# Kernel tuning notes

Hardware: AMD Instinct MI355X
Metric: run time of the kernel (lower is better)

Reference implementation:

```python
import jax, jax.numpy as jnp
import numpy as np

N, E, F, H, L, G = 100000, 1600000, 32, 64, 4, 256
EPS = 1e-5


def setup_inputs() -> dict:
    key = jax.random.key(0)
    ks = jax.random.split(key, 12)
    x = jax.random.normal(ks[0], (N, F), dtype=jnp.float32)
    edge_index = jax.random.randint(ks[1], (2, E), 0, N, dtype=jnp.int32)
    batch = jnp.sort(jax.random.randint(ks[2], (N,), 0, G, dtype=jnp.int32))
    s = 0.1
    return {
        "x": x,
        "edge_index": edge_index,
        "batch": batch,
        "w_embed": jax.random.normal(ks[3], (F, H), dtype=jnp.float32) * s,
        "b_embed": jnp.zeros((H,), dtype=jnp.float32),
        "conv_W": jax.random.normal(ks[4], (L, H, H), dtype=jnp.float32) * s,
        "conv_b": jnp.zeros((L, H), dtype=jnp.float32),
        "bn_gamma": jnp.ones((L, H), dtype=jnp.float32),
        "bn_beta": jnp.zeros((L, H), dtype=jnp.float32),
        "w1": jax.random.normal(ks[5], (H, H // 2), dtype=jnp.float32) * s,
        "b1": jnp.zeros((H // 2,), dtype=jnp.float32),
        "w2": jax.random.normal(ks[6], (H // 2, 1), dtype=jnp.float32) * s,
        "b2": jnp.zeros((1,), dtype=jnp.float32),
    }


def _gcn_conv(h, src, dst, W, b):
    # PyG GCNConv: add self loops, symmetric D^-1/2 (A+I) D^-1/2 normalization
    hw = h @ W  # [N,H]
    deg = jax.ops.segment_sum(jnp.ones((E,), h.dtype), dst, num_segments=N) + 1.0
    dinv = jax.lax.rsqrt(deg)  # [N]
    msg = hw[src] * (dinv[src] * dinv[dst])[:, None]  # [E,H] gather + scale
    agg = jax.ops.segment_sum(msg, dst, num_segments=N)  # scatter-add
    agg = agg + hw * (dinv * dinv)[:, None]  # self-loop contribution
    return agg + b


def _batchnorm(h, gamma, beta):
    # training-mode BatchNorm1d over the node dimension
    mean = jnp.mean(h, axis=0)
    var = jnp.var(h, axis=0)
    return (h - mean) * jax.lax.rsqrt(var + EPS) * gamma + beta


def reference(x, edge_index, batch, w_embed, b_embed, conv_W, conv_b,
              bn_gamma, bn_beta, w1, b1, w2, b2):
    src, dst = edge_index[0], edge_index[1]
    h = x @ w_embed + b_embed  # node embedding [N,H]
    for i in range(L):
        identity = h
        h = _gcn_conv(h, src, dst, conv_W[i], conv_b[i])
        h = _batchnorm(h, bn_gamma[i], bn_beta[i])
        h = jax.nn.relu(h)
        # dropout is identity in eval mode
        h = h + identity  # use_residual=True
    # global mean pool over graphs
    sums = jax.ops.segment_sum(h, batch, num_segments=G)  # [G,H]
    counts = jax.ops.segment_sum(jnp.ones((N,), h.dtype), batch, num_segments=G)
    pooled = sums / jnp.maximum(counts, 1.0)[:, None]
    out = jax.nn.relu(pooled @ w1 + b1)
    out = out @ w2 + b2  # [G,1]
    return out
```

## Files before the change

kernel.cpp:

```cpp
#include <hip/hip_runtime.h>
#include <hip/hip_fp16.h>

#define Nn 100000
#define Ne 1600000
#define Fi 32
#define Hd 64
#define Ll 4
#define Gg 256
#define BN_EPS 1e-5f
#define NPB 128
#define NBINS ((Nn + NPB - 1) / NPB)
#define CHUNK 4096
#define NBLK ((Ne + CHUNK - 1) / CHUNK)
#define IDXW (NBINS + 2)
#define BSLOT 4096
#define TPAD 68
#define XPAD 36
#define NGB ((Nn + 63) / 64)
#define NSH 128


__global__ __launch_bounds__(256) void k_part(const int* __restrict__ src,
                                              const int* __restrict__ dst,
                                              unsigned* __restrict__ tpack,
                                              unsigned short* __restrict__ idx16) {
    __shared__ int hist[NBINS];
    __shared__ int lofs[NBINS + 1];
    __shared__ int wsum[256];
    __shared__ unsigned stage[CHUNK];
    int blk = blockIdx.x, t = threadIdx.x;
    int e0 = blk * CHUNK;
    int nval = min(CHUNK, Ne - e0);

    for (int i = t; i < NBINS; i += 256) hist[i] = 0;
    __syncthreads();
    for (int i = t; i < nval; i += 256)
        atomicAdd(&hist[dst[e0 + i] >> 7], 1);
    __syncthreads();

    int base = t * 4;
    int loc[4];
    int s = 0;
#pragma unroll
    for (int k = 0; k < 4; k++) {
        int b = base + k;
        int c = (b < NBINS) ? hist[b] : 0;
        loc[k] = s;
        s += c;
    }
    wsum[t] = s;
    __syncthreads();
    int x = s;
    for (int off = 1; off < 256; off <<= 1) {
        int u = (t >= off) ? wsum[t - off] : 0;
        __syncthreads();
        x += u;
        wsum[t] = x;
        __syncthreads();
    }
    int excl = x - s;
#pragma unroll
    for (int k = 0; k < 4; k++) {
        int b = base + k;
        if (b < NBINS) lofs[b] = excl + loc[k];
    }
    if (t == 0) lofs[NBINS] = nval;
    __syncthreads();

    for (int i = t; i <= NBINS; i += 256)
        idx16[(size_t)blk * IDXW + i] = (unsigned short)lofs[i];

    for (int i = t; i < NBINS; i += 256) hist[i] = lofs[i];
    __syncthreads();
    for (int i = t; i < nval; i += 256) {
        int d = dst[e0 + i];
        int sv = src[e0 + i];
        int p = atomicAdd(&hist[d >> 7], 1);
        stage[p] = (unsigned)sv | ((unsigned)(d & (NPB - 1)) << 17);
    }
    __syncthreads();
    for (int i = t; i < nval; i += 256)
        tpack[(size_t)blk * CHUNK + i] = stage[i];
}

__global__ __launch_bounds__(512) void k_csr2(const unsigned* __restrict__ tpack,
                                              const unsigned short* __restrict__ idx16,
                                              const int* __restrict__ batch,
                                              int* __restrict__ esrc,
                                              int* __restrict__ row_off,
                                              int* __restrict__ rdeg,
                                              float* __restrict__ dinv,
                                              int* __restrict__ gstart) {
    int t = threadIdx.x;
    if (blockIdx.x == NBINS) {
        if (t < Gg) {
            int lo = 0, hi = Nn;
            while (lo < hi) {
                int mid = (lo + hi) >> 1;
                if (batch[mid] < t) lo = mid + 1; else hi = mid;
            }
            gstart[t] = lo;
            if (t == 0) gstart[Gg] = Nn;
        }
        return;
    }
    __shared__ unsigned edges[BSLOT];
    __shared__ unsigned ordered[BSLOT];
    __shared__ int rlen[512];
    __shared__ int cnt[NPB], startv[NPB], cur[NPB];
    int b = blockIdx.x;
    int n0 = b * NPB;
    int base = b * BSLOT;

    int len = 0, s0 = 0;
    if (t < NBLK) {
        const unsigned short* row = idx16 + (size_t)t * IDXW;
        s0 = row[b];
        len = (int)row[b + 1] - s0;
    }
    rlen[t] = len;
    __syncthreads();
    int x = len;
    for (int off = 1; off < 512; off <<= 1) {
        int u = (t >= off) ? rlen[t - off] : 0;
        __syncthreads();
        x += u;
        rlen[t] = x;
        __syncthreads();
    }
    int lput = x - len;
    int total = rlen[511];
    if (t < NBLK && len > 0) {
        const unsigned* tp = tpack + (size_t)t * CHUNK + s0;
        for (int k = 0; k < len; k++)
            edges[lput + k] = tp[k];
    }
    if (t < NPB) cnt[t] = 0;
    __syncthreads();
    for (int i = t; i < total; i += 512)
        atomicAdd(&cnt[edges[i] >> 17], 1);
    __syncthreads();
    if (t < NPB) startv[t] = cnt[t];
    __syncthreads();
    for (int off = 1; off < NPB; off <<= 1) {
        int u = (t < NPB && t >= off) ? startv[t - off] : 0;
        __syncthreads();
        if (t < NPB) startv[t] += u;
        __syncthreads();
    }
    if (t < NPB) {
        int st = startv[t] - cnt[t];
        cur[t] = st;
        int node = n0 + t;
        if (node < Nn) {
            row_off[node] = base + st;
            rdeg[node] = cnt[t];
            dinv[node] = rsqrtf((float)cnt[t] + 1.0f);
        }
    }
    __syncthreads();
    for (int i = t; i < total; i += 512) {
        unsigned v = edges[i];
        int p = atomicAdd(&cur[v >> 17], 1);
        ordered[p] = v & 0x1FFFFu;
    }
    __syncthreads();
    for (int i = t; i < total; i += 512)
        esrc[base + i] = (int)ordered[i];
}


#define MT_FMA(AV, W0, W1, W2, W3, R)                                          \
    acc[R][0] = fmaf(AV.x, W0.x, acc[R][0]);                                   \
    acc[R][0] = fmaf(AV.y, W1.x, acc[R][0]);                                   \
    acc[R][0] = fmaf(AV.z, W2.x, acc[R][0]);                                   \
    acc[R][0] = fmaf(AV.w, W3.x, acc[R][0]);                                   \
    acc[R][1] = fmaf(AV.x, W0.y, acc[R][1]);                                   \
    acc[R][1] = fmaf(AV.y, W1.y, acc[R][1]);                                   \
    acc[R][1] = fmaf(AV.z, W2.y, acc[R][1]);                                   \
    acc[R][1] = fmaf(AV.w, W3.y, acc[R][1]);                                   \
    acc[R][2] = fmaf(AV.x, W0.z, acc[R][2]);                                   \
    acc[R][2] = fmaf(AV.y, W1.z, acc[R][2]);                                   \
    acc[R][2] = fmaf(AV.z, W2.z, acc[R][2]);                                   \
    acc[R][2] = fmaf(AV.w, W3.z, acc[R][2]);                                   \
    acc[R][3] = fmaf(AV.x, W0.w, acc[R][3]);                                   \
    acc[R][3] = fmaf(AV.y, W1.w, acc[R][3]);                                   \
    acc[R][3] = fmaf(AV.z, W2.w, acc[R][3]);                                   \
    acc[R][3] = fmaf(AV.w, W3.w, acc[R][3]);

__device__ inline void store_half4(unsigned short* dst, float a, float b,
                                   float c, float d) {
    __half2 p0 = __floats2half2_rn(a, b);
    __half2 p1 = __floats2half2_rn(c, d);
    uint2 u;
    u.x = *(unsigned*)&p0;
    u.y = *(unsigned*)&p1;
    *(uint2*)dst = u;
}

__device__ inline void store_half8(unsigned short* dst, const float* a) {
    __half2 p0 = __floats2half2_rn(a[0], a[1]);
    __half2 p1 = __floats2half2_rn(a[2], a[3]);
    __half2 p2 = __floats2half2_rn(a[4], a[5]);
    __half2 p3 = __floats2half2_rn(a[6], a[7]);
    uint4 u;
    u.x = *(unsigned*)&p0; u.y = *(unsigned*)&p1;
    u.z = *(unsigned*)&p2; u.w = *(unsigned*)&p3;
    *(uint4*)dst = u;
}

__device__ inline float4 load_half4(const unsigned short* p) {
    uint2 u = *(const uint2*)p;
    float2 f0 = __half22float2(*(__half2*)&u.x);
    float2 f1 = __half22float2(*(__half2*)&u.y);
    return make_float4(f0.x, f0.y, f1.x, f1.y);
}

__global__ __launch_bounds__(256, 4) void k_gemmF2(const unsigned short* __restrict__ aggh,
                                                   const float* __restrict__ bnacc,
                                                   const float* __restrict__ gamma,
                                                   const float* __restrict__ beta,
                                                   unsigned short* __restrict__ hh,
                                                   const float* __restrict__ W,
                                                   const float* __restrict__ dinv,
                                                   unsigned short* __restrict__ hwh) {
    __shared__ float hs[64 * TPAD];
    __shared__ float ws[64 * 64];
    __shared__ float bsc[64], bsh[64];
    int t = threadIdx.x;
    int n0 = blockIdx.x * 64;

    for (int f = t; f < 1024; f += 256)
        ((float4*)ws)[f] = ((const float4*)W)[f];

    if (t < 64) {
        float s = 0.f, s2 = 0.f;
        for (int shd = 0; shd < NSH; shd++) {
            s  += bnacc[shd * 128 + t];
            s2 += bnacc[shd * 128 + 64 + t];
        }
        float mean = s / (float)Nn;
        float var = fmaxf(s2 / (float)Nn - mean * mean, 0.f);
        float scv = gamma[t] * rsqrtf(var + BN_EPS);
        bsc[t] = scv;
        bsh[t] = beta[t] - mean * scv;
    }
    __syncthreads();

    for (int f = t; f < 1024; f += 256) {
        int row = f >> 4, c4 = (f & 15) * 4;
        int node = n0 + row;
        if (node < Nn) {
            float4 a  = load_half4(aggh + (size_t)node * Hd + c4);
            float4 ho = load_half4(hh + (size_t)node * Hd + c4);
            float4 sc = ((const float4*)bsc)[f & 15];
            float4 sh = ((const float4*)bsh)[f & 15];
            float4 r4;
            r4.x = fmaxf(fmaf(a.x, sc.x, sh.x), 0.f) + ho.x;
            r4.y = fmaxf(fmaf(a.y, sc.y, sh.y), 0.f) + ho.y;
            r4.z = fmaxf(fmaf(a.z, sc.z, sh.z), 0.f) + ho.z;
            r4.w = fmaxf(fmaf(a.w, sc.w, sh.w), 0.f) + ho.w;
            store_half4(hh + (size_t)node * Hd + c4, r4.x, r4.y, r4.z, r4.w);
            *(float4*)&hs[row * TPAD + c4] = r4;
        } else {
            *(float4*)&hs[row * TPAD + c4] = make_float4(0.f, 0.f, 0.f, 0.f);
        }
    }
    __syncthreads();

    int i = t >> 4, j = t & 15;
    float acc[4][4] = {};
#pragma unroll 2
    for (int k = 0; k < 64; k += 4) {
        float4 w0 = *(const float4*)&ws[(k + 0) * 64 + 4 * j];
        float4 w1 = *(const float4*)&ws[(k + 1) * 64 + 4 * j];
        float4 w2 = *(const float4*)&ws[(k + 2) * 64 + 4 * j];
        float4 w3 = *(const float4*)&ws[(k + 3) * 64 + 4 * j];
        float4 a0 = *(const float4*)&hs[(4 * i + 0) * TPAD + k];
        float4 a1 = *(const float4*)&hs[(4 * i + 1) * TPAD + k];
        float4 a2 = *(const float4*)&hs[(4 * i + 2) * TPAD + k];
        float4 a3 = *(const float4*)&hs[(4 * i + 3) * TPAD + k];
        MT_FMA(a0, w0, w1, w2, w3, 0)
        MT_FMA(a1, w0, w1, w2, w3, 1)
        MT_FMA(a2, w0, w1, w2, w3, 2)
        MT_FMA(a3, w0, w1, w2, w3, 3)
    }
#pragma unroll
    for (int r = 0; r < 4; r++) {
        int node = n0 + 4 * i + r;
        if (node < Nn) {
            float dv = dinv[node];
            store_half4(hwh + (size_t)node * Hd + 4 * j,
                        acc[r][0] * dv, acc[r][1] * dv, acc[r][2] * dv,
                        acc[r][3] * dv);
        }
    }
}

__global__ __launch_bounds__(256, 4) void k_embed_gemm2(const float* __restrict__ x,
                                                        const float* __restrict__ we,
                                                        const float* __restrict__ be,
                                                        const float* __restrict__ W,
                                                        unsigned short* __restrict__ hh,
                                                        const float* __restrict__ dinv,
                                                        unsigned short* __restrict__ hwh) {
    __shared__ float uni[64 * XPAD + 32 * 64];
    __shared__ float hs[64 * TPAD];
    __shared__ float bes[64];
    float* xs  = uni;
    float* wes = uni + 64 * XPAD;
    float* ws  = uni;
    int t = threadIdx.x;
    int n0 = blockIdx.x * 64;

    for (int f = t; f < 512; f += 256)
        ((float4*)wes)[f] = ((const float4*)we)[f];
    if (t < 64) bes[t] = be[t];

    for (int f = t; f < 512; f += 256) {
        int row = f >> 3, c4 = (f & 7) * 4;
        int node = n0 + row;
        float4 v = (node < Nn) ? *(const float4*)(x + (size_t)node * Fi + c4)
                               : make_float4(0.f, 0.f, 0.f, 0.f);
        *(float4*)&xs[row * XPAD + c4] = v;
    }
    __syncthreads();

    int i = t >> 4, j = t & 15;
    {
        float acc[4][4];
#pragma unroll
        for (int r = 0; r < 4; r++)
#pragma unroll
            for (int c = 0; c < 4; c++) acc[r][c] = bes[4 * j + c];
#pragma unroll 2
        for (int k = 0; k < 32; k += 4) {
            float4 w0 = *(const float4*)&wes[(k + 0) * 64 + 4 * j];
            float4 w1 = *(const float4*)&wes[(k + 1) * 64 + 4 * j];
            float4 w2 = *(const float4*)&wes[(k + 2) * 64 + 4 * j];
            float4 w3 = *(const float4*)&wes[(k + 3) * 64 + 4 * j];
            float4 a0 = *(const float4*)&xs[(4 * i + 0) * XPAD + k];
            float4 a1 = *(const float4*)&xs[(4 * i + 1) * XPAD + k];
            float4 a2 = *(const float4*)&xs[(4 * i + 2) * XPAD + k];
            float4 a3 = *(const float4*)&xs[(4 * i + 3) * XPAD + k];
            MT_FMA(a0, w0, w1, w2, w3, 0)
            MT_FMA(a1, w0, w1, w2, w3, 1)
            MT_FMA(a2, w0, w1, w2, w3, 2)
            MT_FMA(a3, w0, w1, w2, w3, 3)
        }
#pragma unroll
        for (int r = 0; r < 4; r++) {
            int node = n0 + 4 * i + r;
            float4 hv = make_float4(acc[r][0], acc[r][1], acc[r][2], acc[r][3]);
            *(float4*)&hs[(4 * i + r) * TPAD + 4 * j] = hv;
            if (node < Nn)
                store_half4(hh + (size_t)node * Hd + 4 * j, hv.x, hv.y, hv.z, hv.w);
        }
    }
    __syncthreads();
    for (int f = t; f < 1024; f += 256)
        ((float4*)ws)[f] = ((const float4*)W)[f];
    __syncthreads();
    {
        float acc[4][4] = {};
#pragma unroll 2
        for (int k = 0; k < 64; k += 4) {
            float4 w0 = *(const float4*)&ws[(k + 0) * 64 + 4 * j];
            float4 w1 = *(const float4*)&ws[(k + 1) * 64 + 4 * j];
            float4 w2 = *(const float4*)&ws[(k + 2) * 64 + 4 * j];
            float4 w3 = *(const float4*)&ws[(k + 3) * 64 + 4 * j];
            float4 a0 = *(const float4*)&hs[(4 * i + 0) * TPAD + k];
            float4 a1 = *(const float4*)&hs[(4 * i + 1) * TPAD + k];
            float4 a2 = *(const float4*)&hs[(4 * i + 2) * TPAD + k];
            float4 a3 = *(const float4*)&hs[(4 * i + 3) * TPAD + k];
            MT_FMA(a0, w0, w1, w2, w3, 0)
            MT_FMA(a1, w0, w1, w2, w3, 1)
            MT_FMA(a2, w0, w1, w2, w3, 2)
            MT_FMA(a3, w0, w1, w2, w3, 3)
        }
#pragma unroll
        for (int r = 0; r < 4; r++) {
            int node = n0 + 4 * i + r;
            if (node < Nn) {
                float dv = dinv[node];
                store_half4(hwh + (size_t)node * Hd + 4 * j,
                            acc[r][0] * dv, acc[r][1] * dv, acc[r][2] * dv,
                            acc[r][3] * dv);
            }
        }
    }
}


__global__ __launch_bounds__(256) void k_gatherH(const unsigned short* __restrict__ hwh,
                                                 const float* __restrict__ dinv,
                                                 const int* __restrict__ row_off,
                                                 const int* __restrict__ rdeg,
                                                 const int* __restrict__ esrc,
                                                 const float* __restrict__ bias,
                                                 unsigned short* __restrict__ aggh,
                                                 float* __restrict__ bnacc) {
    int g = threadIdx.x >> 3;
    int l = threadIdx.x & 7;
    int node = blockIdx.x * 32 + g;
    float di = dinv[node];
    float acc[8];

    uint4 v = *(const uint4*)(hwh + (size_t)node * Hd + l * 8);
#pragma unroll
    for (int q = 0; q < 4; q++) {
        float2 f = __half22float2(*(__half2*)(((unsigned*)&v) + q));
        acc[2 * q]     = f.x;
        acc[2 * q + 1] = f.y;
    }

    int e = row_off[node];
    int e1 = e + rdeg[node];
    for (; e + 7 < e1; e += 8) {
        uint4 vv[8];
#pragma unroll
        for (int u = 0; u < 8; u++)
            vv[u] = *(const uint4*)(hwh + (size_t)esrc[e + u] * Hd + l * 8);
#pragma unroll
        for (int u = 0; u < 8; u++) {
#pragma unroll
            for (int q = 0; q < 4; q++) {
                float2 f = __half22float2(*(__half2*)(((unsigned*)&vv[u]) + q));
                acc[2 * q]     += f.x;
                acc[2 * q + 1] += f.y;
            }
        }
    }
    for (; e + 1 < e1; e += 2) {
        uint4 v0 = *(const uint4*)(hwh + (size_t)esrc[e] * Hd + l * 8);
        uint4 v1 = *(const uint4*)(hwh + (size_t)esrc[e + 1] * Hd + l * 8);
#pragma unroll
        for (int q = 0; q < 4; q++) {
            float2 f0 = __half22float2(*(__half2*)(((unsigned*)&v0) + q));
            float2 f1 = __half22float2(*(__half2*)(((unsigned*)&v1) + q));
            acc[2 * q]     += f0.x + f1.x;
            acc[2 * q + 1] += f0.y + f1.y;
        }
    }
    if (e < e1) {
        uint4 v0 = *(const uint4*)(hwh + (size_t)esrc[e] * Hd + l * 8);
#pragma unroll
        for (int q = 0; q < 4; q++) {
            float2 f0 = __half22float2(*(__half2*)(((unsigned*)&v0) + q));
            acc[2 * q]     += f0.x;
            acc[2 * q + 1] += f0.y;
        }
    }

#pragma unroll
    for (int q = 0; q < 8; q++)
        acc[q] = fmaf(acc[q], di, bias[l * 8 + q]);

    store_half8(aggh + (size_t)node * Hd + l * 8, acc);

    __shared__ float ls[2048];
    *(float4*)&ls[g * 64 + l * 8]     = make_float4(acc[0], acc[1], acc[2], acc[3]);
    *(float4*)&ls[g * 64 + l * 8 + 4] = make_float4(acc[4], acc[5], acc[6], acc[7]);
    __syncthreads();
    int t = threadIdx.x;
    if (t < 64) {
        float s = 0.f, s2 = 0.f;
#pragma unroll
        for (int gg = 0; gg < 32; gg++) {
            float vv = ls[gg * 64 + t];
            s += vv;
            s2 = fmaf(vv, vv, s2);
        }
        float* a = bnacc + (blockIdx.x & (NSH - 1)) * 128;
        atomicAdd(&a[t], s);
        atomicAdd(&a[64 + t], s2);
    }
}

__global__ __launch_bounds__(1024) void k_poolF(const unsigned short* __restrict__ aggh,
                                                const float* __restrict__ bnacc,
                                                const float* __restrict__ gamma,
                                                const float* __restrict__ beta,
                                                const unsigned short* __restrict__ hh,
                                                const int* __restrict__ gstart,
                                                float* __restrict__ pooled) {
    __shared__ float ls[1024];
    __shared__ float bsc[64], bsh[64];
    int g = blockIdx.x;
    int t = threadIdx.x;
    if (t < 64) {
        float s = 0.f, s2 = 0.f;
        for (int shd = 0; shd < NSH; shd++) {
            s  += bnacc[shd * 128 + t];
            s2 += bnacc[shd * 128 + 64 + t];
        }
        float mean = s / (float)Nn;
        float var = fmaxf(s2 / (float)Nn - mean * mean, 0.f);
        float scv = gamma[t] * rsqrtf(var + BN_EPS);
        bsc[t] = scv;
        bsh[t] = beta[t] - mean * scv;
    }
    __syncthreads();
    int ch = t & 63, sl = t >> 6;
    float sc = bsc[ch], shv = bsh[ch];
    int n0 = gstart[g], n1 = gstart[g + 1];
    float s = 0.f;
    for (int n = n0 + sl; n < n1; n += 16) {
        float a  = __half2float(((const __half*)aggh)[(size_t)n * Hd + ch]);
        float ho = __half2float(((const __half*)hh)[(size_t)n * Hd + ch]);
        s += fmaxf(fmaf(a, sc, shv), 0.f) + ho;
    }
    ls[t] = s;
    __syncthreads();
    if (t < 64) {
        float acc = 0.f;
#pragma unroll
        for (int k = 0; k < 16; k++) acc += ls[k * 64 + t];
        float cnt = (float)(n1 - n0);
        pooled[g * Hd + t] = acc / fmaxf(cnt, 1.0f);
    }
}

__global__ __launch_bounds__(256) void k_head(const float* __restrict__ pooled,
                                              const float* __restrict__ w1,
                                              const float* __restrict__ b1,
                                              const float* __restrict__ w2,
                                              const float* __restrict__ b2,
                                              float* __restrict__ out) {
    __shared__ float sw1[Hd * 32], sw2[32], sb1[32];
    int t = threadIdx.x;
    for (int i = t; i < Hd * 32; i += 256) sw1[i] = w1[i];
    if (t < 32) { sw2[t] = w2[t]; sb1[t] = b1[t]; }
    __syncthreads();
    float acc2[32];
#pragma unroll
    for (int k = 0; k < 32; k++) acc2[k] = sb1[k];
    for (int j = 0; j < Hd; j++) {
        float pj = pooled[t * Hd + j];
#pragma unroll
        for (int k = 0; k < 32; k++) acc2[k] = fmaf(pj, sw1[j * 32 + k], acc2[k]);
    }
    float o = b2[0];
#pragma unroll
    for (int k = 0; k < 32; k++) o += fmaxf(acc2[k], 0.f) * sw2[k];
    out[t] = o;
}


extern "C" void kernel_launch(void* const* d_in, const int* in_sizes, int n_in,
                              void* d_out, int out_size, void* d_ws, size_t ws_size,
                              hipStream_t stream) {
    const float* x       = (const float*)d_in[0];
    const int*   eidx    = (const int*)d_in[1];
    const int*   batch   = (const int*)d_in[2];
    const float* w_embed = (const float*)d_in[3];
    const float* b_embed = (const float*)d_in[4];
    const float* conv_W  = (const float*)d_in[5];
    const float* conv_b  = (const float*)d_in[6];
    const float* gamma   = (const float*)d_in[7];
    const float* beta    = (const float*)d_in[8];
    const float* w1      = (const float*)d_in[9];
    const float* b1      = (const float*)d_in[10];
    const float* w2      = (const float*)d_in[11];
    const float* b2      = (const float*)d_in[12];
    const int* src = eidx;
    const int* dst = eidx + Ne;

    char* p = (char*)d_ws;
    auto alloc = [&](size_t bytes) -> void* {
        void* r = (void*)p;
        p += (bytes + 255) / 256 * 256;
        return r;
    };
    unsigned short* hh  = (unsigned short*)alloc((size_t)Nn * Hd * 2);
    unsigned short* hwh = (unsigned short*)alloc((size_t)Nn * Hd * 2);
    unsigned short* aggh = (unsigned short*)alloc((size_t)Nn * Hd * 2);
    int*      row_off = (int*)alloc((size_t)Nn * 4);
    int*      rdeg    = (int*)alloc((size_t)Nn * 4);
    float*    dinv    = (float*)alloc((size_t)Nn * 4);
    int*      esrc    = (int*)alloc((size_t)NBINS * BSLOT * 4);
    unsigned* tpack   = (unsigned*)alloc((size_t)NBLK * CHUNK * 4);
    unsigned short* idx16 = (unsigned short*)alloc((size_t)NBLK * IDXW * 2);
    float*    bnacc   = (float*)alloc((size_t)Ll * NSH * 128 * 4);
    float*    pooled  = (float*)alloc((size_t)Gg * Hd * 4);
    int*      gstart  = (int*)alloc((size_t)(Gg + 1) * 4);
    (void)ws_size; (void)in_sizes; (void)n_in; (void)out_size;

    const int NB_G32 = Nn / 32;

    hipMemsetAsync(bnacc, 0, (size_t)Ll * NSH * 128 * 4, stream);

    k_part<<<NBLK, 256, 0, stream>>>(src, dst, tpack, idx16);
    k_csr2<<<NBINS + 1, 512, 0, stream>>>(tpack, idx16, batch, esrc, row_off,
                                          rdeg, dinv, gstart);

    k_embed_gemm2<<<NGB, 256, 0, stream>>>(x, w_embed, b_embed, conv_W, hh, dinv, hwh);

    for (int i = 0; i < Ll; i++) {
        if (i > 0)
            k_gemmF2<<<NGB, 256, 0, stream>>>(aggh, bnacc + (size_t)(i - 1) * NSH * 128,
                                              gamma + (size_t)(i - 1) * Hd,
                                              beta + (size_t)(i - 1) * Hd, hh,
                                              conv_W + (size_t)i * Hd * Hd, dinv, hwh);
        k_gatherH<<<NB_G32, 256, 0, stream>>>(hwh, dinv, row_off, rdeg, esrc,
                                              conv_b + (size_t)i * Hd, aggh,
                                              bnacc + (size_t)i * NSH * 128);
    }

    k_poolF<<<Gg, 1024, 0, stream>>>(aggh, bnacc + (size_t)(Ll - 1) * NSH * 128,
                                     gamma + (size_t)(Ll - 1) * Hd,
                                     beta + (size_t)(Ll - 1) * Hd, hh, gstart, pooled);
    k_head<<<1, 256, 0, stream>>>(pooled, w1, b1, w2, b2, (float*)d_out);
}
```

Baseline: 293.6 us.

## Degree-sort nodes for gather load balance and cache dst in LDS

Adds a three-kernel counting sort that buckets nodes by in-degree (capped at 63) into a permutation. The gather kernel then processes nodes in that order, so the nodes sharing a wavefront have similar edge counts and lanes diverge less in the edge loop. Separately, the partition kernel now stages dst indices in shared memory instead of reading them from global memory twice. In exchange it adds three small launches, and output rows and self-feature reads become non-contiguous across each block.

```diff
diff --git a/kernel.cpp b/kernel.cpp
--- a/kernel.cpp
+++ b/kernel.cpp
@@ -18,6 +18,7 @@
 #define XPAD 36
 #define NGB ((Nn + 63) / 64)
 #define NSH 128
+#define NB_N ((Nn + 255) / 256)
 
 
 __global__ __launch_bounds__(256) void k_part(const int* __restrict__ src,
@@ -28,14 +29,16 @@
     __shared__ int lofs[NBINS + 1];
     __shared__ int wsum[256];
     __shared__ unsigned stage[CHUNK];
+    __shared__ int dbuf[CHUNK];
     int blk = blockIdx.x, t = threadIdx.x;
     int e0 = blk * CHUNK;
     int nval = min(CHUNK, Ne - e0);
 
     for (int i = t; i < NBINS; i += 256) hist[i] = 0;
+    for (int i = t; i < nval; i += 256) dbuf[i] = dst[e0 + i];
     __syncthreads();
     for (int i = t; i < nval; i += 256)
-        atomicAdd(&hist[dst[e0 + i] >> 7], 1);
+        atomicAdd(&hist[dbuf[i] >> 7], 1);
     __syncthreads();
 
     int base = t * 4;
@@ -73,7 +76,7 @@
     for (int i = t; i < NBINS; i += 256) hist[i] = lofs[i];
     __syncthreads();
     for (int i = t; i < nval; i += 256) {
-        int d = dst[e0 + i];
+        int d = dbuf[i];
         int sv = src[e0 + i];
         int p = atomicAdd(&hist[d >> 7], 1);
         stage[p] = (unsigned)sv | ((unsigned)(d & (NPB - 1)) << 17);
@@ -170,6 +173,64 @@
 }
 
 
+__global__ __launch_bounds__(256) void k_sortA(const int* __restrict__ rdeg,
+                                               int* __restrict__ gh) {
+    __shared__ int lh[64];
+    int t = threadIdx.x, b = blockIdx.x;
+    if (t < 64) lh[t] = 0;
+    __syncthreads();
+    int i = b * 256 + t;
+    if (i < Nn) atomicAdd(&lh[min(rdeg[i], 63)], 1);
+    __syncthreads();
+    if (t < 64 && lh[t])
+        atomicAdd(&gh[(b & 63) * 64 + t], lh[t]);
+}
+
+__global__ __launch_bounds__(512) void k_sortB(int* __restrict__ gh) {
+    __shared__ int part[512];
+    int t = threadIdx.x;
+    int s0 = t * 8;
+    int loc[8];
+    int sum = 0;
+#pragma unroll
+    for (int k = 0; k < 8; k++) {
+        int seq = s0 + k;
+        int bin = seq >> 6, shard = seq & 63;
+        loc[k] = sum;
+        sum += gh[shard * 64 + bin];
+    }
+    part[t] = sum;
+    __syncthreads();
+    int x = sum;
+    for (int off = 1; off < 512; off <<= 1) {
+        int u = (t >= off) ? part[t - off] : 0;
+        __syncthreads();
+        x += u;
+        part[t] = x;
+        __syncthreads();
+    }
+    int excl = x - sum;
+#pragma unroll
+    for (int k = 0; k < 8; k++) {
+        int seq = s0 + k;
+        int bin = seq >> 6, shard = seq & 63;
+        gh[shard * 64 + bin] = excl + loc[k];
+    }
+}
+
+__global__ __launch_bounds__(256) void k_sortC(const int* __restrict__ rdeg,
+                                               int* __restrict__ gh,
+                                               int* __restrict__ perm) {
+    int t = threadIdx.x, b = blockIdx.x;
+    int i = b * 256 + t;
+    if (i < Nn) {
+        int bin = min(rdeg[i], 63);
+        int pos = atomicAdd(&gh[(b & 63) * 64 + bin], 1);
+        perm[pos] = i;
+    }
+}
+
+
 #define MT_FMA(AV, W0, W1, W2, W3, R)                                          \
     acc[R][0] = fmaf(AV.x, W0.x, acc[R][0]);                                   \
     acc[R][0] = fmaf(AV.y, W1.x, acc[R][0]);                                   \
@@ -397,12 +458,13 @@
                                                  const int* __restrict__ row_off,
                                                  const int* __restrict__ rdeg,
                                                  const int* __restrict__ esrc,
+                                                 const int* __restrict__ perm,
                                                  const float* __restrict__ bias,
                                                  unsigned short* __restrict__ aggh,
                                                  float* __restrict__ bnacc) {
     int g = threadIdx.x >> 3;
     int l = threadIdx.x & 7;
-    int node = blockIdx.x * 32 + g;
+    int node = perm[blockIdx.x * 32 + g];
     float di = dinv[node];
     float acc[8];
 
@@ -578,9 +640,11 @@
     int*      row_off = (int*)alloc((size_t)Nn * 4);
     int*      rdeg    = (int*)alloc((size_t)Nn * 4);
     float*    dinv    = (float*)alloc((size_t)Nn * 4);
+    int*      perm    = (int*)alloc((size_t)Nn * 4);
     int*      esrc    = (int*)alloc((size_t)NBINS * BSLOT * 4);
     unsigned* tpack   = (unsigned*)alloc((size_t)NBLK * CHUNK * 4);
     unsigned short* idx16 = (unsigned short*)alloc((size_t)NBLK * IDXW * 2);
+    int*      gh      = (int*)alloc(64 * 64 * 4);
     float*    bnacc   = (float*)alloc((size_t)Ll * NSH * 128 * 4);
     float*    pooled  = (float*)alloc((size_t)Gg * Hd * 4);
     int*      gstart  = (int*)alloc((size_t)(Gg + 1) * 4);
@@ -588,11 +652,14 @@
 
     const int NB_G32 = Nn / 32;
 
-    hipMemsetAsync(bnacc, 0, (size_t)Ll * NSH * 128 * 4, stream);
+    hipMemsetAsync(gh, 0, 64 * 64 * 4 + (size_t)Ll * NSH * 128 * 4, stream);
 
     k_part<<<NBLK, 256, 0, stream>>>(src, dst, tpack, idx16);
     k_csr2<<<NBINS + 1, 512, 0, stream>>>(tpack, idx16, batch, esrc, row_off,
                                           rdeg, dinv, gstart);
+    k_sortA<<<NB_N, 256, 0, stream>>>(rdeg, gh);
+    k_sortB<<<1, 512, 0, stream>>>(gh);
+    k_sortC<<<NB_N, 256, 0, stream>>>(rdeg, gh, perm);
 
     k_embed_gemm2<<<NGB, 256, 0, stream>>>(x, w_embed, b_embed, conv_W, hh, dinv, hwh);
 
@@ -602,7 +669,7 @@
                                               gamma + (size_t)(i - 1) * Hd,
                                               beta + (size_t)(i - 1) * Hd, hh,
                                               conv_W + (size_t)i * Hd * Hd, dinv, hwh);
-        k_gatherH<<<NB_G32, 256, 0, stream>>>(hwh, dinv, row_off, rdeg, esrc,
+        k_gatherH<<<NB_G32, 256, 0, stream>>>(hwh, dinv, row_off, rdeg, esrc, perm,
                                               conv_b + (size_t)i * Hd, aggh,
                                               bnacc + (size_t)i * NSH * 128);
     }
```

Result: slower. 310.7 us (+5.8%).
